# Optimization experiments

Hardware: AMD Instinct MI355X
Metric: run time of the kernel (lower is better)

Reference implementation:

```python
import jax, jax.numpy as jnp
import numpy as np

N_NODES = 100000
N_EDGES = 3200000
IN_FEAT = 128


def gcn_conv(x, src, dst, W, b, num_nodes):
    # PyG GCNConv: h = x @ W, then symmetric-normalized aggregation with self-loops.
    h = x @ W  # [N, out]
    # add self loops
    loop = jnp.arange(num_nodes, dtype=src.dtype)
    s = jnp.concatenate([src, loop])
    d = jnp.concatenate([dst, loop])
    # degree over destination (col) with unit edge weights
    deg = jax.ops.segment_sum(jnp.ones_like(s, dtype=h.dtype), d, num_segments=num_nodes)
    dinv = jnp.where(deg > 0, jax.lax.rsqrt(deg), 0.0)
    norm = dinv[s] * dinv[d]  # [E+N]
    msg = norm[:, None] * h[s]  # gather source features, scale per edge
    out = jax.ops.segment_sum(msg, d, num_segments=num_nodes)
    return out + b


def setup_inputs() -> dict:
    key = jax.random.key(0)
    ks = jax.random.split(key, 8)
    x = jax.random.normal(ks[0], (N_NODES, IN_FEAT), dtype=jnp.float32)
    edge_index = jax.random.randint(ks[1], (2, N_EDGES), 0, N_NODES, dtype=jnp.int64)
    def glorot(k, shape):
        lim = np.sqrt(6.0 / (shape[0] + shape[1]))
        return jax.random.uniform(k, shape, jnp.float32, -lim, lim)
    return {
        "x": x,
        "edge_index": edge_index,
        "W1": glorot(ks[2], (IN_FEAT, 4)), "b1": jnp.zeros((4,), jnp.float32),
        "W2": glorot(ks[3], (4, 2)),       "b2": jnp.zeros((2,), jnp.float32),
        "W3": glorot(ks[4], (2, 1)),       "b3": jnp.zeros((1,), jnp.float32),
    }


def reference(x, edge_index, W1, b1, W2, b2, W3, b3):
    src, dst = edge_index[0], edge_index[1]
    n = x.shape[0]
    h = gcn_conv(x, src, dst, W1, b1, n)
    h = jax.nn.relu(h)
    # F.dropout(training=self.training): inference mode -> identity
    h = gcn_conv(h, src, dst, W2, b2, n)
    h = jax.nn.relu(h)
    h = gcn_conv(h, src, dst, W3, b3, n)
    return jax.nn.sigmoid(h)  # [N, 1]
```

## Files before the change

### kernel.cpp

```cpp
#include <hip/hip_runtime.h>
#include <hip/hip_bf16.h>
#include <math.h>


#define TPB 256
#define CHUNK 4096
#define EPT (CHUNK / TPB)
#define SLAB2 9216

__global__ __launch_bounds__(TPB) void k_hist(const int* __restrict__ dst,
                                              int* __restrict__ histT,
                                              int NS, int NB, int E) {
    __shared__ int h[512];
    int t = threadIdx.x;
    h[t] = 0; h[t + 256] = 0;
    __syncthreads();
    int base = blockIdx.x * CHUNK, end = min(base + CHUNK, E);
    for (int e = base + t; e < end; e += TPB) atomicAdd(&h[dst[e] >> 8], 1);
    __syncthreads();
    for (int i = t; i < NB; i += TPB) histT[(size_t)i * NS + blockIdx.x] = h[i];
}

__global__ __launch_bounds__(TPB) void k_scanA(int* __restrict__ histT,
                                               int* __restrict__ binTotal, int NS) {
    __shared__ int s[TPB];
    int* row = histT + (size_t)blockIdx.x * NS;
    int t = threadIdx.x;
    int run = 0;
    for (int base = 0; base < NS; base += TPB) {
        int i = base + t;
        int v = (i < NS) ? row[i] : 0;
        s[t] = v;
        __syncthreads();
        int x = v;
        for (int d = 1; d < TPB; d <<= 1) {
            int y = (t >= d) ? s[t - d] : 0;
            __syncthreads();
            x += y; s[t] = x;
            __syncthreads();
        }
        if (i < NS) row[i] = run + (x - v);
        run += s[TPB - 1];
        __syncthreads();
    }
    if (t == 0) binTotal[blockIdx.x] = run;
}

__global__ __launch_bounds__(512) void k_scanB(const int* __restrict__ binTotal,
                                               int* __restrict__ binBase, int NB) {
    __shared__ int s[512];
    int t = threadIdx.x;
    int v = (t < NB) ? binTotal[t] : 0;
    s[t] = v;
    __syncthreads();
    int x = v;
    for (int d = 1; d < 512; d <<= 1) {
        int y = (t >= d) ? s[t - d] : 0;
        __syncthreads();
        x += y; s[t] = x;
        __syncthreads();
    }
    if (t < NB) binBase[t] = x - v;
}

__global__ __launch_bounds__(TPB) void k_sortscatter(
    const int* __restrict__ src, const int* __restrict__ dst,
    const int* __restrict__ histT, const int* __restrict__ binBase,
    unsigned int* __restrict__ pairs2, int NS, int NB, int E)
{
    __shared__ int hist[512];
    __shared__ int s[TPB];
    __shared__ int gbase[512];
    __shared__ unsigned int sorted[CHUNK];
    int t = threadIdx.x, blk = blockIdx.x;
    int base = blk * CHUNK;
    int n = min(CHUNK, E - base);
    hist[t] = 0; hist[t + 256] = 0;
    for (int i = t; i < NB; i += TPB)
        gbase[i] = binBase[i] + histT[(size_t)i * NS + blk];
    __syncthreads();
    unsigned int meta[EPT];
#pragma unroll
    for (int k = 0; k < EPT; ++k) {
        int li = k * TPB + t;
        if (li < n) {
            int d = dst[base + li];
            int lp = atomicAdd(&hist[d >> 8], 1);
            meta[k] = ((unsigned)d << 13) | (unsigned)lp;
        } else meta[k] = 0xFFFFFFFFu;
    }
    __syncthreads();
    int run = 0;
    for (int cb = 0; cb < 512; cb += TPB) {
        int v = hist[cb + t];
        s[t] = v;
        __syncthreads();
        int x = v;
        for (int d = 1; d < TPB; d <<= 1) {
            int y = (t >= d) ? s[t - d] : 0;
            __syncthreads();
            x += y; s[t] = x;
            __syncthreads();
        }
        hist[cb + t] = run + (x - v);
        run += s[TPB - 1];
        __syncthreads();
    }
#pragma unroll
    for (int k = 0; k < EPT; ++k) {
        if (meta[k] != 0xFFFFFFFFu) {
            unsigned m = meta[k];
            int d = (int)(m >> 13);
            int lp = (int)(m & 0x1FFFu);
            unsigned p = (unsigned)src[base + k * TPB + t] | ((unsigned)(d & 255) << 17);
            sorted[hist[d >> 8] + lp] = p;
        }
    }
    __syncthreads();
    int grp = t >> 4, ln = t & 15;
    for (int b = grp; b < NB; b += 16) {
        int ls = hist[b];
        int len = hist[b + 1] - ls;
        int go = gbase[b];
        for (int k = ln; k < len; k += 16) pairs2[go + k] = sorted[ls + k];
    }
}

__global__ __launch_bounds__(TPB) void k_degree2(
    unsigned int* __restrict__ pairs2, const int* __restrict__ binBase,
    const int* __restrict__ binTotal, int* __restrict__ cnt,
    int* __restrict__ off, float* __restrict__ dinv,
    float* __restrict__ hs1, int N)
{
    __shared__ unsigned int pl[SLAB2];
    __shared__ int c[TPB], s[TPB], cur[TPB];
    int t = threadIdx.x, b = blockIdx.x;
    int base = binBase[b];
    int total = min(binTotal[b], SLAB2);
    c[t] = 0;
    __syncthreads();
    for (int i = t; i < total; i += TPB) pl[i] = pairs2[base + i];
    __syncthreads();
    for (int i = t; i < total; i += TPB) atomicAdd(&c[(pl[i] >> 17) & 255], 1);
    __syncthreads();
    int cv = c[t];
    s[t] = cv;
    __syncthreads();
    int x = cv;
    for (int d = 1; d < TPB; d <<= 1) {
        int y = (t >= d) ? s[t - d] : 0;
        __syncthreads();
        x += y; s[t] = x;
        __syncthreads();
    }
    int excl = x - cv;
    int v = (b << 8) + t;
    if (v < N) {
        cnt[v] = cv;
        off[v] = base + excl;
        float di = rsqrtf((float)(cv + 1));
        dinv[v] = di;
        float4 h = ((float4*)hs1)[v];
        ((float4*)hs1)[v] = make_float4(di * h.x, di * h.y, di * h.z, di * h.w);
    }
    cur[t] = excl;
    __syncthreads();
    for (int i = t; i < total; i += TPB) {
        unsigned p = pl[i];
        int pos = atomicAdd(&cur[(p >> 17) & 255], 1);
        pairs2[base + pos] = p & 0x1FFFFu;
    }
}

__global__ __launch_bounds__(TPB) void k_node1(
    const float* __restrict__ x, const float* __restrict__ W1,
    float* __restrict__ hs1, int n) {
    __shared__ float Ws[512];
    for (int i = threadIdx.x; i < 512; i += TPB) Ws[i] = W1[i];
    __syncthreads();
    int t = blockIdx.x * TPB + threadIdx.x;
    int v = t >> 2, p = t & 3;
    if (v >= n) return;
    const float4* xr = (const float4*)(x + (size_t)v * 128);
    float a0 = 0.f, a1 = 0.f, a2 = 0.f, a3 = 0.f;
#pragma unroll
    for (int i = 0; i < 8; ++i) {
        int c = p + i * 4;
        float4 xx = xr[c];
        const float* w = &Ws[c * 16];
        a0 += xx.x * w[0] + xx.y * w[4] + xx.z * w[8]  + xx.w * w[12];
        a1 += xx.x * w[1] + xx.y * w[5] + xx.z * w[9]  + xx.w * w[13];
        a2 += xx.x * w[2] + xx.y * w[6] + xx.z * w[10] + xx.w * w[14];
        a3 += xx.x * w[3] + xx.y * w[7] + xx.z * w[11] + xx.w * w[15];
    }
    a0 += __shfl_xor(a0, 1); a0 += __shfl_xor(a0, 2);
    a1 += __shfl_xor(a1, 1); a1 += __shfl_xor(a1, 2);
    a2 += __shfl_xor(a2, 1); a2 += __shfl_xor(a2, 2);
    a3 += __shfl_xor(a3, 1); a3 += __shfl_xor(a3, 2);
    if (p == 0) ((float4*)hs1)[v] = make_float4(a0, a1, a2, a3);
}

__global__ __launch_bounds__(TPB) void k_gather1(
    const int* __restrict__ off, const int* __restrict__ cnt,
    const int* __restrict__ ssrc, const float* __restrict__ hs1,
    const float* __restrict__ dinv, const float* __restrict__ b1,
    const float* __restrict__ W2, float* __restrict__ hs2, int n) {
    int t = blockIdx.x * TPB + threadIdx.x;
    int v = t >> 3, p = t & 7;
    if (v >= n) return;
    int base = off[v], c = cnt[v];
    float4 acc = make_float4(0.f, 0.f, 0.f, 0.f);
    for (int i = p; i < c; i += 8) {
        int s = ssrc[base + i];
        float4 h = ((const float4*)hs1)[s];
        acc.x += h.x; acc.y += h.y; acc.z += h.z; acc.w += h.w;
    }
    acc.x += __shfl_xor(acc.x, 1); acc.x += __shfl_xor(acc.x, 2); acc.x += __shfl_xor(acc.x, 4);
    acc.y += __shfl_xor(acc.y, 1); acc.y += __shfl_xor(acc.y, 2); acc.y += __shfl_xor(acc.y, 4);
    acc.z += __shfl_xor(acc.z, 1); acc.z += __shfl_xor(acc.z, 2); acc.z += __shfl_xor(acc.z, 4);
    acc.w += __shfl_xor(acc.w, 1); acc.w += __shfl_xor(acc.w, 2); acc.w += __shfl_xor(acc.w, 4);
    if (p == 0) {
        float4 hv = ((const float4*)hs1)[v];
        float di = dinv[v];
        float o0 = fmaxf(di * (acc.x + hv.x) + b1[0], 0.f);
        float o1 = fmaxf(di * (acc.y + hv.y) + b1[1], 0.f);
        float o2 = fmaxf(di * (acc.z + hv.z) + b1[2], 0.f);
        float o3 = fmaxf(di * (acc.w + hv.w) + b1[3], 0.f);
        float h0 = o0 * W2[0] + o1 * W2[2] + o2 * W2[4] + o3 * W2[6];
        float h1 = o0 * W2[1] + o1 * W2[3] + o2 * W2[5] + o3 * W2[7];
        ((float2*)hs2)[v] = make_float2(di * h0, di * h1);
    }
}

__global__ __launch_bounds__(TPB) void k_gather2(
    const int* __restrict__ off, const int* __restrict__ cnt,
    const int* __restrict__ ssrc, const float* __restrict__ hs2,
    const float* __restrict__ dinv, const float* __restrict__ b2,
    const float* __restrict__ W3, float* __restrict__ hs3, int n) {
    int t = blockIdx.x * TPB + threadIdx.x;
    int v = t >> 3, p = t & 7;
    if (v >= n) return;
    int base = off[v], c = cnt[v];
    float2 acc = make_float2(0.f, 0.f);
    for (int i = p; i < c; i += 8) {
        int s = ssrc[base + i];
        float2 h = ((const float2*)hs2)[s];
        acc.x += h.x; acc.y += h.y;
    }
    acc.x += __shfl_xor(acc.x, 1); acc.x += __shfl_xor(acc.x, 2); acc.x += __shfl_xor(acc.x, 4);
    acc.y += __shfl_xor(acc.y, 1); acc.y += __shfl_xor(acc.y, 2); acc.y += __shfl_xor(acc.y, 4);
    if (p == 0) {
        float2 hv = ((const float2*)hs2)[v];
        float di = dinv[v];
        float o0 = fmaxf(di * (acc.x + hv.x) + b2[0], 0.f);
        float o1 = fmaxf(di * (acc.y + hv.y) + b2[1], 0.f);
        float h3 = o0 * W3[0] + o1 * W3[1];
        hs3[v] = di * h3;
    }
}

__global__ __launch_bounds__(TPB) void k_gather3(
    const int* __restrict__ off, const int* __restrict__ cnt,
    const int* __restrict__ ssrc, const float* __restrict__ hs3,
    const float* __restrict__ dinv, const float* __restrict__ b3,
    float* __restrict__ out, int n) {
    int t = blockIdx.x * TPB + threadIdx.x;
    int v = t >> 3, p = t & 7;
    if (v >= n) return;
    int base = off[v], c = cnt[v];
    float acc = 0.f;
    for (int i = p; i < c; i += 8) acc += hs3[ssrc[base + i]];
    acc += __shfl_xor(acc, 1); acc += __shfl_xor(acc, 2); acc += __shfl_xor(acc, 4);
    if (p == 0) {
        float di = dinv[v];
        float agg = di * (acc + hs3[v]) + b3[0];
        out[v] = 1.0f / (1.0f + __expf(-agg));
    }
}

extern "C" void kernel_launch(void* const* d_in, const int* in_sizes, int n_in,
                              void* d_out, int out_size, void* d_ws, size_t ws_size,
                              hipStream_t stream) {
    const float* x  = (const float*)d_in[0];
    const int* ei   = (const int*)d_in[1];
    const float* W1 = (const float*)d_in[2];
    const float* b1 = (const float*)d_in[3];
    const float* W2 = (const float*)d_in[4];
    const float* b2 = (const float*)d_in[5];
    const float* W3 = (const float*)d_in[6];
    const float* b3 = (const float*)d_in[7];
    float* out = (float*)d_out;

    const int N = in_sizes[0] / 128;
    const int E = in_sizes[1] / 2;
    const int* src = ei;
    const int* dst = ei + E;

    const int NS = (E + CHUNK - 1) / CHUNK;
    const int NB = (N + 255) >> 8;

    char* w = (char*)d_ws;
    auto carve = [&](size_t bytes) { char* p = w; w += (bytes + 15) & ~(size_t)15; return p; };
    int* histT           = (int*)carve((size_t)NB * NS * 4);
    int* binTotal        = (int*)carve((size_t)NB * 4);
    int* binBase         = (int*)carve((size_t)NB * 4);
    unsigned int* pairs2 = (unsigned int*)carve((size_t)E * 4);
    int* cnt             = (int*)carve((size_t)N * 4);
    int* off             = (int*)carve((size_t)N * 4);
    float* dinv          = (float*)carve((size_t)N * 4);
    float* hs1           = (float*)carve((size_t)N * 16);
    float* hs2           = (float*)carve((size_t)N * 8);
    float* hs3           = (float*)carve((size_t)N * 4);

    const int nbN4 = (4 * N + TPB - 1) / TPB;
    const int nbN8 = (8 * N + TPB - 1) / TPB;

    k_hist       <<<NS, TPB, 0, stream>>>(dst, histT, NS, NB, E);
    k_scanA      <<<NB, TPB, 0, stream>>>(histT, binTotal, NS);
    k_scanB      <<<1, 512, 0, stream>>>(binTotal, binBase, NB);
    k_node1      <<<nbN4, TPB, 0, stream>>>(x, W1, hs1, N);
    k_sortscatter<<<NS, TPB, 0, stream>>>(src, dst, histT, binBase, pairs2, NS, NB, E);
    k_degree2    <<<NB, TPB, 0, stream>>>(pairs2, binBase, binTotal, cnt, off, dinv, hs1, N);
    k_gather1    <<<nbN8, TPB, 0, stream>>>(off, cnt, (const int*)pairs2, hs1, dinv, b1, W2, hs2, N);
    k_gather2    <<<nbN8, TPB, 0, stream>>>(off, cnt, (const int*)pairs2, hs2, dinv, b2, W3, hs3, N);
    k_gather3    <<<nbN8, TPB, 0, stream>>>(off, cnt, (const int*)pairs2, hs3, dinv, b3, out, N);
}
```

Measured before the change: 232.4 us.

## Split edge bucketing into local partition pass and global placement pass

The separate histogram kernel is replaced by a partition kernel. It sorts each 4096-edge chunk by destination bin in shared memory once, then writes the locally sorted chunk, per-bin local starts and bin counts to workspace. A new placement kernel reloads each sorted chunk with vector loads and copies each bin segment to its global offset, using 8 lanes per bin instead of 16. This removes the recomputation of the local sort and scan in the scatter stage. In exchange it adds a full extra write and read of a chunk-sized slab through global memory.

Measured after the change: 227.2 us. 2.3% less time.

```diff
diff --git a/kernel.cpp b/kernel.cpp
--- a/kernel.cpp
+++ b/kernel.cpp
@@ -8,23 +8,70 @@
 #define EPT (CHUNK / TPB)
 #define SLAB2 9216
 
-__global__ __launch_bounds__(TPB) void k_hist(const int* __restrict__ dst,
-                                              int* __restrict__ histT,
-                                              int NS, int NB, int E) {
-    __shared__ int h[512];
-    int t = threadIdx.x;
-    h[t] = 0; h[t + 256] = 0;
-    __syncthreads();
-    int base = blockIdx.x * CHUNK, end = min(base + CHUNK, E);
-    for (int e = base + t; e < end; e += TPB) atomicAdd(&h[dst[e] >> 8], 1);
-    __syncthreads();
-    for (int i = t; i < NB; i += TPB) histT[(size_t)i * NS + blockIdx.x] = h[i];
-}
-
-__global__ __launch_bounds__(TPB) void k_scanA(int* __restrict__ histT,
+__global__ __launch_bounds__(TPB) void k_part(
+    const int* __restrict__ src, const int* __restrict__ dst,
+    unsigned int* __restrict__ slab, int* __restrict__ lstart,
+    int* __restrict__ cntT, int NS, int NB, int NBP, int E)
+{
+    __shared__ int hist[512];
+    __shared__ int s[TPB];
+    __shared__ unsigned int sorted[CHUNK];
+    int t = threadIdx.x, blk = blockIdx.x;
+    int base = blk * CHUNK;
+    int n = min(CHUNK, E - base);
+    hist[t] = 0; hist[t + 256] = 0;
+    __syncthreads();
+    unsigned int meta[EPT];
+#pragma unroll
+    for (int k = 0; k < EPT; ++k) {
+        int li = k * TPB + t;
+        if (li < n) {
+            int d = dst[base + li];
+            int lp = atomicAdd(&hist[d >> 8], 1);
+            meta[k] = ((unsigned)d << 13) | (unsigned)lp;
+        } else meta[k] = 0xFFFFFFFFu;
+    }
+    __syncthreads();
+    for (int i = t; i < NB; i += TPB) cntT[(size_t)i * NS + blk] = hist[i];
+    __syncthreads();
+    int run = 0;
+    for (int cb = 0; cb < 512; cb += TPB) {
+        int v = hist[cb + t];
+        s[t] = v;
+        __syncthreads();
+        int x = v;
+        for (int d = 1; d < TPB; d <<= 1) {
+            int y = (t >= d) ? s[t - d] : 0;
+            __syncthreads();
+            x += y; s[t] = x;
+            __syncthreads();
+        }
+        hist[cb + t] = run + (x - v);
+        run += s[TPB - 1];
+        __syncthreads();
+    }
+#pragma unroll
+    for (int k = 0; k < EPT; ++k) {
+        if (meta[k] != 0xFFFFFFFFu) {
+            unsigned m = meta[k];
+            int d = (int)(m >> 13);
+            int lp = (int)(m & 0x1FFFu);
+            unsigned p = (unsigned)src[base + k * TPB + t] | ((unsigned)(d & 255) << 17);
+            sorted[hist[d >> 8] + lp] = p;
+        }
+    }
+    __syncthreads();
+    const uint4* s4 = (const uint4*)sorted;
+    uint4* g4 = (uint4*)(slab + (size_t)base);
+    for (int i = t; i < CHUNK / 4; i += TPB) g4[i] = s4[i];
+    for (int i = t; i < NBP; i += TPB)
+        lstart[(size_t)blk * NBP + i] = (i < NB) ? hist[i] : n;
+}
+
+__global__ __launch_bounds__(TPB) void k_scanA(int* __restrict__ cntT,
                                                int* __restrict__ binTotal, int NS) {
     __shared__ int s[TPB];
-    int* row = histT + (size_t)blockIdx.x * NS;
+    int* row = cntT + (size_t)blockIdx.x * NS;
     int t = threadIdx.x;
     int run = 0;
     for (int base = 0; base < NS; base += TPB) {
@@ -63,66 +110,29 @@
     if (t < NB) binBase[t] = x - v;
 }
 
-__global__ __launch_bounds__(TPB) void k_sortscatter(
-    const int* __restrict__ src, const int* __restrict__ dst,
-    const int* __restrict__ histT, const int* __restrict__ binBase,
-    unsigned int* __restrict__ pairs2, int NS, int NB, int E)
+__global__ __launch_bounds__(TPB) void k_place(
+    const unsigned int* __restrict__ slab, const int* __restrict__ lstart,
+    const int* __restrict__ cntT ,
+    const int* __restrict__ binBase, unsigned int* __restrict__ pairs2,
+    int NS, int NB, int NBP)
 {
-    __shared__ int hist[512];
-    __shared__ int s[TPB];
-    __shared__ int gbase[512];
-    __shared__ unsigned int sorted[CHUNK];
+    __shared__ unsigned int ch[CHUNK];
+    __shared__ int lls[512];
+    __shared__ int ddo[512];
     int t = threadIdx.x, blk = blockIdx.x;
-    int base = blk * CHUNK;
-    int n = min(CHUNK, E - base);
-    hist[t] = 0; hist[t + 256] = 0;
+    const uint4* g4 = (const uint4*)(slab + (size_t)blk * CHUNK);
+    uint4* c4 = (uint4*)ch;
+    for (int i = t; i < CHUNK / 4; i += TPB) c4[i] = g4[i];
+    for (int i = t; i < NBP; i += TPB) lls[i] = lstart[(size_t)blk * NBP + i];
     for (int i = t; i < NB; i += TPB)
-        gbase[i] = binBase[i] + histT[(size_t)i * NS + blk];
-    __syncthreads();
-    unsigned int meta[EPT];
-#pragma unroll
-    for (int k = 0; k < EPT; ++k) {
-        int li = k * TPB + t;
-        if (li < n) {
-            int d = dst[base + li];
-            int lp = atomicAdd(&hist[d >> 8], 1);
-            meta[k] = ((unsigned)d << 13) | (unsigned)lp;
-        } else meta[k] = 0xFFFFFFFFu;
-    }
-    __syncthreads();
-    int run = 0;
-    for (int cb = 0; cb < 512; cb += TPB) {
-        int v = hist[cb + t];
-        s[t] = v;
-        __syncthreads();
-        int x = v;
-        for (int d = 1; d < TPB; d <<= 1) {
-            int y = (t >= d) ? s[t - d] : 0;
-            __syncthreads();
-            x += y; s[t] = x;
-            __syncthreads();
-        }
-        hist[cb + t] = run + (x - v);
-        run += s[TPB - 1];
-        __syncthreads();
-    }
-#pragma unroll
-    for (int k = 0; k < EPT; ++k) {
-        if (meta[k] != 0xFFFFFFFFu) {
-            unsigned m = meta[k];
-            int d = (int)(m >> 13);
-            int lp = (int)(m & 0x1FFFu);
-            unsigned p = (unsigned)src[base + k * TPB + t] | ((unsigned)(d & 255) << 17);
-            sorted[hist[d >> 8] + lp] = p;
-        }
-    }
-    __syncthreads();
-    int grp = t >> 4, ln = t & 15;
-    for (int b = grp; b < NB; b += 16) {
-        int ls = hist[b];
-        int len = hist[b + 1] - ls;
-        int go = gbase[b];
-        for (int k = ln; k < len; k += 16) pairs2[go + k] = sorted[ls + k];
+        ddo[i] = binBase[i] + cntT[(size_t)i * NS + blk];
+    __syncthreads();
+    int grp = t >> 3, ln = t & 7;
+    for (int b = grp; b < NB; b += 32) {
+        int ls = lls[b];
+        int len = lls[b + 1] - ls;
+        int go = ddo[b];
+        for (int k = ln; k < len; k += 8) pairs2[go + k] = ch[ls + k];
     }
 }
 
@@ -296,12 +306,15 @@
     const int* src = ei;
     const int* dst = ei + E;
 
-    const int NS = (E + CHUNK - 1) / CHUNK;
-    const int NB = (N + 255) >> 8;
+    const int NS  = (E + CHUNK - 1) / CHUNK;
+    const int NB  = (N + 255) >> 8;
+    const int NBP = NB + 1;
 
     char* w = (char*)d_ws;
     auto carve = [&](size_t bytes) { char* p = w; w += (bytes + 15) & ~(size_t)15; return p; };
-    int* histT           = (int*)carve((size_t)NB * NS * 4);
+    unsigned int* slab   = (unsigned int*)carve((size_t)NS * CHUNK * 4);
+    int* lstart          = (int*)carve((size_t)NS * NBP * 4);
+    int* cntT            = (int*)carve((size_t)NB * NS * 4);
     int* binTotal        = (int*)carve((size_t)NB * 4);
     int* binBase         = (int*)carve((size_t)NB * 4);
     unsigned int* pairs2 = (unsigned int*)carve((size_t)E * 4);
@@ -315,13 +328,13 @@
     const int nbN4 = (4 * N + TPB - 1) / TPB;
     const int nbN8 = (8 * N + TPB - 1) / TPB;
 
-    k_hist       <<<NS, TPB, 0, stream>>>(dst, histT, NS, NB, E);
-    k_scanA      <<<NB, TPB, 0, stream>>>(histT, binTotal, NS);
-    k_scanB      <<<1, 512, 0, stream>>>(binTotal, binBase, NB);
-    k_node1      <<<nbN4, TPB, 0, stream>>>(x, W1, hs1, N);
-    k_sortscatter<<<NS, TPB, 0, stream>>>(src, dst, histT, binBase, pairs2, NS, NB, E);
-    k_degree2    <<<NB, TPB, 0, stream>>>(pairs2, binBase, binTotal, cnt, off, dinv, hs1, N);
-    k_gather1    <<<nbN8, TPB, 0, stream>>>(off, cnt, (const int*)pairs2, hs1, dinv, b1, W2, hs2, N);
-    k_gather2    <<<nbN8, TPB, 0, stream>>>(off, cnt, (const int*)pairs2, hs2, dinv, b2, W3, hs3, N);
-    k_gather3    <<<nbN8, TPB, 0, stream>>>(off, cnt, (const int*)pairs2, hs3, dinv, b3, out, N);
-}
+    k_part   <<<NS, TPB, 0, stream>>>(src, dst, slab, lstart, cntT, NS, NB, NBP, E);
+    k_scanA  <<<NB, TPB, 0, stream>>>(cntT, binTotal, NS);
+    k_scanB  <<<1, 512, 0, stream>>>(binTotal, binBase, NB);
+    k_node1  <<<nbN4, TPB, 0, stream>>>(x, W1, hs1, N);
+    k_place  <<<NS, TPB, 0, stream>>>(slab, lstart, cntT, binBase, pairs2, NS, NB, NBP);
+    k_degree2<<<NB, TPB, 0, stream>>>(pairs2, binBase, binTotal, cnt, off, dinv, hs1, N);
+    k_gather1<<<nbN8, TPB, 0, stream>>>(off, cnt, (const int*)pairs2, hs1, dinv, b1, W2, hs2, N);
+    k_gather2<<<nbN8, TPB, 0, stream>>>(off, cnt, (const int*)pairs2, hs2, dinv, b2, W3, hs3, N);
+    k_gather3<<<nbN8, TPB, 0, stream>>>(off, cnt, (const int*)pairs2, hs3, dinv, b3, out, N);
+}
```
